# Kernel optimization log

Measured on AMD Instinct MI355X. Metric: run time of the kernel, lower is better.

## Reference

```python
import jax, jax.numpy as jnp
from jax import lax
import numpy as np

EPS = 1e-5

def _bn(y, g, b):
    # train-mode batchnorm over (B, H, W) per channel, biased variance (torch default)
    m = y.mean(axis=(0, 2, 3), keepdims=True)
    v = y.var(axis=(0, 2, 3), keepdims=True)
    return (y - m) * lax.rsqrt(v + EPS) * g[None, :, None, None] + b[None, :, None, None]

def _pool13(y):
    # max_pool2d kernel (13,1), stride (13,1); torch truncates the remainder
    B, Ch, L, C = y.shape
    L2 = (L // 13) * 13
    return y[:, :, :L2, :].reshape(B, Ch, L // 13, 13, C).max(axis=3)

def _stagenet(x, w1, b1, w2, b2, g1, be1, w3, b3, g2, be2, wl, bl):
    # x: (B, T=3000, C) -> (B, 100)
    B = x.shape[0]
    y = jnp.einsum('btc,oc->bot', x, w1) + b1[None, :, None]   # spatial conv across channels
    y = y.transpose(0, 2, 1)[:, None]                          # (B,1,T,C)
    y = lax.conv_general_dilated(y, w2, (1, 1), 'VALID', dimension_numbers=('NCHW', 'OIHW', 'NCHW')) + b2[None, :, None, None]
    y = _pool13(_bn(jax.nn.relu(y), g1, be1))                  # (B,16,227,C)
    y = lax.conv_general_dilated(y, w3, (1, 1), 'VALID', dimension_numbers=('NCHW', 'OIHW', 'NCHW')) + b3[None, :, None, None]
    y = _pool13(_bn(jax.nn.relu(y), g2, be2))                  # (B,16,13,C)
    return y.reshape(B, -1) @ wl.T + bl                        # (B,100)

def _gru_last(xs, wih, whh, bih, bhh):
    # xs: (B, S, D) -> final hidden state (B, H); torch gate order r, z, n
    h0 = jnp.zeros((xs.shape[0], whh.shape[1]), xs.dtype)
    def step(h, x):
        gi = x @ wih.T + bih
        gh = h @ whh.T + bhh
        ir, iz, inn = jnp.split(gi, 3, axis=-1)
        hr, hz, hnn = jnp.split(gh, 3, axis=-1)
        r = jax.nn.sigmoid(ir + hr)
        z = jax.nn.sigmoid(iz + hz)
        n = jnp.tanh(inn + r * hnn)
        return (1.0 - z) * n + z * h, None
    hT, _ = lax.scan(step, h0, xs.transpose(1, 0, 2))
    return hT

def setup_inputs() -> dict:
    key = jax.random.key(0)
    ks = jax.random.split(key, 16)
    B, Np, Nb, T, C, H = 16, 16, 10, 3000, 2, 100
    s = 0.1
    f32 = jnp.float32
    return {
        'Xc': jax.random.normal(ks[0], (B, Np, T, C), f32),
        'Xp': jax.random.normal(ks[1], (B, Np, T, C), f32),
        'Xb': jax.random.normal(ks[2], (B, Np, Nb, T, C), f32),
        'sn_w1': jax.random.normal(ks[3], (C, C), f32) * s,
        'sn_b1': jnp.zeros((C,), f32),
        'sn_w2': jax.random.normal(ks[4], (16, 1, 50, 1), f32) * s,
        'sn_b2': jnp.zeros((16,), f32),
        'sn_g1': jnp.ones((16,), f32),
        'sn_be1': jnp.zeros((16,), f32),
        'sn_w3': jax.random.normal(ks[5], (16, 16, 50, 1), f32) * s,
        'sn_b3': jnp.zeros((16,), f32),
        'sn_g2': jnp.ones((16,), f32),
        'sn_be2': jnp.zeros((16,), f32),
        'sn_wl': jax.random.normal(ks[6], (H, 16 * 13 * C), f32) * s,
        'sn_bl': jnp.zeros((H,), f32),
        'gru_wih': jax.random.normal(ks[7], (3 * H, H), f32) * s,
        'gru_whh': jax.random.normal(ks[8], (3 * H, H), f32) * s,
        'gru_bih': jnp.zeros((3 * H,), f32),
        'gru_bhh': jnp.zeros((3 * H,), f32),
        'bilin_w': jax.random.normal(ks[9], (Np, H, H), f32) * s,
    }

def reference(Xc, Xp, Xb, sn_w1, sn_b1, sn_w2, sn_b2, sn_g1, sn_be1, sn_w3, sn_b3, sn_g2, sn_be2, sn_wl, sn_bl, gru_wih, gru_whh, gru_bih, gru_bhh, bilin_w):
    sn = lambda x: _stagenet(x, sn_w1, sn_b1, sn_w2, sn_b2, sn_g1, sn_be1, sn_w3, sn_b3, sn_g2, sn_be2, sn_wl, sn_bl)
    B, Np, Nb, T, C = Xb.shape
    # each original stagenet call sees one window with batch B (BN stats per call) -> vmap over windows
    xb = jax.vmap(sn)(Xb.transpose(1, 2, 0, 3, 4).reshape(Np * Nb, B, T, C))
    xb = xb.reshape(Np, Nb, B, -1).transpose(2, 0, 1, 3)            # (B,Np,Nb,100)
    xc = jax.vmap(sn)(Xc.transpose(1, 0, 2, 3)).transpose(1, 0, 2)  # (B,S,100)
    xp = jax.vmap(sn)(Xp.transpose(1, 0, 2, 3)).transpose(1, 0, 2)  # (B,Np,100)
    hn = _gru_last(xc, gru_wih, gru_whh, gru_bih, gru_bhh)          # (B,100)
    cand = jnp.concatenate([xp[:, :, None, :], xb], axis=2)         # (B,Np,Nb+1,100)
    # per-step bilinear scoring: replaces the triple nested loop of nn.Bilinear calls
    return jnp.einsum('bh,phc,bpsc->bps', hn, bilin_w, cand)        # (B,16,11)
```

## Files before the change

kernel.cpp:

```cpp
#include <hip/hip_runtime.h>
#include <hip/hip_bf16.h>


#define NSEQ 3072
#define CNT1 94432.0f
#define CNT2 5696.0f

__global__ __launch_bounds__(256) void k0_prep(
    const float* __restrict__ wl, const float* __restrict__ w3,
    const float* __restrict__ wih, const float* __restrict__ whh,
    float* __restrict__ wlT, float* __restrict__ w3T,
    float* __restrict__ wihT, float* __restrict__ whhT)
{
    int i = blockIdx.x * 256 + threadIdx.x;
    if (i < 41600) { int h = i / 416, c = i - h * 416; wlT[c * 100 + h] = wl[i]; }
    if (i < 12800) { int co = i / 800, r = i - co * 800; int ci = r / 50, k = r - ci * 50;
                     w3T[(ci * 50 + k) * 16 + co] = w3[i]; }
    if (i < 30000) { int j = i / 100, c = i - j * 100;
                     wihT[c * 300 + j] = wih[i]; whhT[c * 300 + j] = whh[i]; }
}

__global__ __launch_bounds__(256) void k1(
    const float* __restrict__ Xc, const float* __restrict__ Xp, const float* __restrict__ Xb,
    const float* __restrict__ w1, const float* __restrict__ b1,
    const float* __restrict__ w2, const float* __restrict__ b2,
    const float* __restrict__ g1,
    float* __restrict__ pooled1, float* __restrict__ bp1)
{
    const int s = blockIdx.x;
    const int g = s >> 4, b = s & 15;
    const float* x;
    if (g < 160)      { int p = g / 10, nb = g - p * 10; x = Xb + (size_t)((b * 16 + p) * 10 + nb) * 6000; }
    else if (g < 176) { int p = g - 160; x = Xc + (size_t)(b * 16 + p) * 6000; }
    else              { int p = g - 176; x = Xp + (size_t)(b * 16 + p) * 6000; }

    __shared__ __align__(16) float u[6000];
    __shared__ float w2s[800];
    __shared__ float red[512];
    const int tid = threadIdx.x;

    for (int i = tid; i < 800; i += 256) w2s[i] = w2[i];
    float w100 = w1[0], w101 = w1[1], w110 = w1[2], w111 = w1[3];
    float b10 = b1[0], b11 = b1[1];
    for (int t4 = tid; t4 < 1500; t4 += 256) {
        float4 xv = ((const float4*)x)[t4];
        float4 uv;
        uv.x = fmaf(xv.y, w101, fmaf(xv.x, w100, b10));
        uv.y = fmaf(xv.y, w111, fmaf(xv.x, w110, b11));
        uv.z = fmaf(xv.w, w101, fmaf(xv.z, w100, b10));
        uv.w = fmaf(xv.w, w111, fmaf(xv.z, w110, b11));
        ((float4*)u)[t4] = uv;
    }
    __syncthreads();

    const int pair = tid & 31, ch = pair >> 1, col = pair & 1, w8 = tid >> 5;
    float wk[50];
    #pragma unroll
    for (int k = 0; k < 50; ++k) wk[k] = w2s[ch * 50 + k];
    #pragma unroll
    for (int k = 0; k < 50; ++k) asm volatile("" : "+v"(wk[k]));
    const float bias = b2[ch];
    const bool useMax = (g1[ch] >= 0.0f);

    float lsum = 0.0f, lsq = 0.0f;
    #pragma unroll 1
    for (int w = w8; w < 227; w += 8) {
        const int t0 = w * 13;
        float acc[13];
        #pragma unroll
        for (int j = 0; j < 13; ++j) acc[j] = bias;
        #pragma unroll
        for (int tk = 0; tk < 62; ++tk) {
            float uv = u[(t0 + tk) * 2 + col];
            const int jlo = (tk > 49) ? (tk - 49) : 0;
            const int jhi = (tk < 12) ? tk : 12;
            #pragma unroll
            for (int j = 0; j < 13; ++j)
                if (j >= jlo && j <= jhi) acc[j] = fmaf(uv, wk[tk - j], acc[j]);
        }
        float sel = useMax ? -1e30f : 1e30f;
        #pragma unroll
        for (int j = 0; j < 13; ++j) {
            float r = fmaxf(acc[j], 0.0f);
            lsum += r; lsq = fmaf(r, r, lsq);
            sel = useMax ? fmaxf(sel, r) : fminf(sel, r);
        }
        pooled1[(size_t)s * 7264 + (size_t)w * 32 + pair] = sel;
    }

    red[tid] = lsum;
    __syncthreads();
    float partial_sq = lsq;
    if (tid < 16) {
        float a = 0.0f;
        for (int t = 0; t < 16; ++t) { int idx = (t >> 1) * 32 + tid * 2 + (t & 1); a += red[idx]; }
        bp1[(s * 16 + tid) * 2 + 0] = a;
    }
    __syncthreads();
    red[tid] = partial_sq;
    __syncthreads();
    if (tid < 16) {
        float q = 0.0f;
        for (int t = 0; t < 16; ++t) { int idx = (t >> 1) * 32 + tid * 2 + (t & 1); q += red[idx]; }
        bp1[(s * 16 + tid) * 2 + 1] = q;
    }
}

__global__ __launch_bounds__(448) void k2(
    const float* __restrict__ pooled1, const float* __restrict__ bp1,
    const float* __restrict__ g1, const float* __restrict__ be1,
    const float* __restrict__ w3T, const float* __restrict__ b3,
    const float* __restrict__ g2,
    float* __restrict__ pooled2, float* __restrict__ bp2)
{
    const int s = blockIdx.x, g = s >> 4;
    __shared__ float in2[7424];
    __shared__ float w3b[2][800];
    __shared__ float sc1[16], sh1[16];
    __shared__ float red[896];
    const int tid = threadIdx.x;

    if (tid < 16) {
        float sum = 0.0f, sq = 0.0f;
        for (int sb = 0; sb < 16; ++sb) {
            const float* pp = &bp1[((g * 16 + sb) * 16 + tid) * 2];
            sum += pp[0]; sq += pp[1];
        }
        float m = sum * (1.0f / CNT1);
        float v = sq * (1.0f / CNT1) - m * m;
        float scv = g1[tid] * rsqrtf(v + 1e-5f);
        sc1[tid] = scv; sh1[tid] = be1[tid] - m * scv;
    }
    if (tid < 160) { int row = tid / 5, w = 227 + tid % 5; in2[row * 232 + w] = 0.0f; }
    for (int i = tid; i < 800; i += 448) w3b[0][i] = w3T[i];
    __syncthreads();
    for (int idx = tid; idx < 7264; idx += 448) {
        int w = idx >> 5, pr = idx & 31, ch = pr >> 1, cl = pr & 1;
        in2[(cl * 16 + ch) * 232 + w] = fmaf(pooled1[(size_t)s * 7264 + idx], sc1[ch], sh1[ch]);
    }

    const int pair = tid & 31, co = pair >> 1, col = pair & 1, wslot = tid >> 5;
    const int t0 = wslot * 13;
    float acc[13];
    const float bias = b3[co];
    #pragma unroll
    for (int j = 0; j < 13; ++j) acc[j] = bias;
    __syncthreads();

    for (int ci = 0; ci < 16; ++ci) {
        const int cur = ci & 1;
        if (ci < 15)
            for (int i = tid; i < 800; i += 448) w3b[cur ^ 1][i] = w3T[(ci + 1) * 800 + i];
        float wk[50];
        #pragma unroll
        for (int k = 0; k < 50; ++k) wk[k] = w3b[cur][k * 16 + co];
        #pragma unroll
        for (int k = 0; k < 50; ++k) asm volatile("" : "+v"(wk[k]));
        const float* ip = &in2[(col * 16 + ci) * 232 + t0];
        #pragma unroll
        for (int tk = 0; tk < 62; ++tk) {
            float uv = ip[tk];
            const int jlo = (tk > 49) ? (tk - 49) : 0;
            const int jhi = (tk < 12) ? tk : 12;
            #pragma unroll
            for (int j = 0; j < 13; ++j)
                if (j >= jlo && j <= jhi) acc[j] = fmaf(uv, wk[tk - j], acc[j]);
        }
        __syncthreads();
    }

    float lsum = 0.0f, lsq = 0.0f;
    const bool useMax2 = (g2[co] >= 0.0f);
    float sel = useMax2 ? -1e30f : 1e30f;
    {
        const int base = wslot * 13;
        #pragma unroll
        for (int j = 0; j < 13; ++j) {
            if (base + j < 178) {
                float r = fmaxf(acc[j], 0.0f);
                lsum += r; lsq = fmaf(r, r, lsq);
                sel = useMax2 ? fmaxf(sel, r) : fminf(sel, r);
            }
        }
        if (wslot < 13) pooled2[(size_t)s * 416 + co * 26 + wslot * 2 + col] = sel;
    }
    red[tid] = lsum; red[448 + tid] = lsq;
    __syncthreads();
    if (tid < 16) {
        float a = 0.0f, q = 0.0f;
        for (int t = 0; t < 28; ++t) {
            int idx = (t >> 1) * 32 + tid * 2 + (t & 1);
            a += red[idx]; q += red[448 + idx];
        }
        bp2[(s * 16 + tid) * 2 + 0] = a;
        bp2[(s * 16 + tid) * 2 + 1] = q;
    }
}

__global__ __launch_bounds__(128) void k3(
    const float* __restrict__ bp2, const float* __restrict__ g2, const float* __restrict__ be2,
    const float* __restrict__ pooled2, const float* __restrict__ wlT,
    const float* __restrict__ bl, float* __restrict__ feat)
{
    const int s = blockIdx.x, g = s >> 4;
    const int tid = threadIdx.x;
    __shared__ float sc[16], sh[16], z[416];
    if (tid < 16) {
        float sum = 0.0f, sq = 0.0f;
        for (int sb = 0; sb < 16; ++sb) {
            const float* pp = &bp2[((g * 16 + sb) * 16 + tid) * 2];
            sum += pp[0]; sq += pp[1];
        }
        float m = sum * (1.0f / CNT2);
        float v = sq * (1.0f / CNT2) - m * m;
        float scv = g2[tid] * rsqrtf(v + 1e-5f);
        sc[tid] = scv; sh[tid] = be2[tid] - m * scv;
    }
    __syncthreads();
    for (int i = tid; i < 416; i += 128) {
        int co = i / 26;
        z[i] = fmaf(pooled2[(size_t)s * 416 + i], sc[co], sh[co]);
    }
    __syncthreads();
    for (int h = tid; h < 100; h += 128) {
        float acc = bl[h];
        for (int i = 0; i < 416; ++i) acc = fmaf(wlT[i * 100 + h], z[i], acc);
        feat[(size_t)s * 100 + h] = acc;
    }
}

__global__ __launch_bounds__(128) void k4a(
    const float* __restrict__ feat, const float* __restrict__ wihT,
    const float* __restrict__ bih, float* __restrict__ gi)
{
    const int b = blockIdx.x >> 4, p = blockIdx.x & 15;
    const int tid = threadIdx.x;
    __shared__ float xr[100];
    if (tid < 100) xr[tid] = feat[(size_t)((160 + p) * 16 + b) * 100 + tid];
    __syncthreads();
    for (int j = tid; j < 300; j += 128) {
        float acc = bih[j];
        for (int i = 0; i < 100; ++i) acc = fmaf(xr[i], wihT[i * 300 + j], acc);
        gi[(size_t)(b * 16 + p) * 300 + j] = acc;
    }
}

__global__ __launch_bounds__(320) void k4b(
    const float* __restrict__ gi, const float* __restrict__ whhT,
    const float* __restrict__ bhh, float* __restrict__ hn)
{
    const int b = blockIdx.x;
    const int tid = threadIdx.x;
    __shared__ float h[100], ga[300], gb[300];
    if (tid < 100) h[tid] = 0.0f;
    __syncthreads();
    for (int p = 0; p < 16; ++p) {
        if (tid < 300) {
            float acc = bhh[tid];
            for (int i = 0; i < 100; ++i) acc = fmaf(h[i], whhT[i * 300 + tid], acc);
            gb[tid] = acc;
            ga[tid] = gi[(size_t)(b * 16 + p) * 300 + tid];
        }
        __syncthreads();
        if (tid < 100) {
            float r  = 1.0f / (1.0f + expf(-(ga[tid] + gb[tid])));
            float zz = 1.0f / (1.0f + expf(-(ga[100 + tid] + gb[100 + tid])));
            float n  = tanhf(ga[200 + tid] + r * gb[200 + tid]);
            h[tid] = (1.0f - zz) * n + zz * h[tid];
        }
        __syncthreads();
    }
    if (tid < 100) hn[b * 100 + tid] = h[tid];
}

__global__ __launch_bounds__(128) void k5(
    const float* __restrict__ hn, const float* __restrict__ bw,
    const float* __restrict__ feat, float* __restrict__ out)
{
    const int b = blockIdx.x >> 4, p = blockIdx.x & 15;
    const int tid = threadIdx.x;
    __shared__ float hs[100], ts[100];
    if (tid < 100) hs[tid] = hn[b * 100 + tid];
    __syncthreads();
    if (tid < 100) {
        float acc = 0.0f;
        for (int hh = 0; hh < 100; ++hh)
            acc = fmaf(hs[hh], bw[(size_t)(p * 100 + hh) * 100 + tid], acc);
        ts[tid] = acc;
    }
    __syncthreads();
    if (tid < 11) {
        const float* cr = (tid == 0)
            ? &feat[(size_t)((176 + p) * 16 + b) * 100]
            : &feat[(size_t)((p * 10 + tid - 1) * 16 + b) * 100];
        float acc = 0.0f;
        for (int hh = 0; hh < 100; ++hh) acc = fmaf(ts[hh], cr[hh], acc);
        out[(b * 16 + p) * 11 + tid] = acc;
    }
}

extern "C" void kernel_launch(void* const* d_in, const int* in_sizes, int n_in,
                              void* d_out, int out_size, void* d_ws, size_t ws_size,
                              hipStream_t stream) {
    (void)in_sizes; (void)n_in; (void)out_size; (void)ws_size;
    const float* Xc  = (const float*)d_in[0];
    const float* Xp  = (const float*)d_in[1];
    const float* Xb  = (const float*)d_in[2];
    const float* w1  = (const float*)d_in[3];
    const float* b1  = (const float*)d_in[4];
    const float* w2  = (const float*)d_in[5];
    const float* b2  = (const float*)d_in[6];
    const float* g1  = (const float*)d_in[7];
    const float* be1 = (const float*)d_in[8];
    const float* w3  = (const float*)d_in[9];
    const float* b3  = (const float*)d_in[10];
    const float* g2  = (const float*)d_in[11];
    const float* be2 = (const float*)d_in[12];
    const float* wl  = (const float*)d_in[13];
    const float* bl  = (const float*)d_in[14];
    const float* wih = (const float*)d_in[15];
    const float* whh = (const float*)d_in[16];
    const float* bih = (const float*)d_in[17];
    const float* bhh = (const float*)d_in[18];
    const float* bw  = (const float*)d_in[19];

    float* ws      = (float*)d_ws;
    float* bp1     = ws;
    float* bp2     = ws + 98304;
    float* wlT     = ws + 196608;
    float* w3T     = ws + 238208;
    float* wihT    = ws + 251008;
    float* whhT    = ws + 281008;
    float* gi      = ws + 311008;
    float* hn      = ws + 387808;
    float* feat    = ws + 389408;
    float* pooled2 = ws + 696608;
    float* pooled1 = ws + 1974560;

    k0_prep<<<163, 256, 0, stream>>>(wl, w3, wih, whh, wlT, w3T, wihT, whhT);
    k1<<<NSEQ, 256, 0, stream>>>(Xc, Xp, Xb, w1, b1, w2, b2, g1, pooled1, bp1);
    k2<<<NSEQ, 448, 0, stream>>>(pooled1, bp1, g1, be1, w3T, b3, g2, pooled2, bp2);
    k3<<<NSEQ, 128, 0, stream>>>(bp2, g2, be2, pooled2, wlT, bl, feat);
    k4a<<<256, 128, 0, stream>>>(feat, wihT, bih, gi);
    k4b<<<16, 320, 0, stream>>>(gi, whhT, bhh, hn);
    k5<<<256, 128, 0, stream>>>(hn, bw, feat, (float*)d_out);
}
```

Baseline: 804.4 us.

## Restructure k2 to 256 threads with two output windows per thread

The second conv kernel now runs with 256 threads instead of 448, and each thread computes up to two pooled windows (slot w8 and w8+8), so weights loaded into registers are reused across both windows. The transposed w3 layout becomes per-output-channel contiguous with padding to 52, which lets each thread read its 50 weights as a contiguous run from shared memory. The asm register-pinning barriers are dropped in k1 and k2, and k2 gets launch_bounds(256,2). This trades more per-thread register pressure and imbalance (only 6 of 8 warps do the second window) for fewer threads and better weight reuse.

```diff
diff --git a/kernel.cpp b/kernel.cpp
--- a/kernel.cpp
+++ b/kernel.cpp
@@ -15,7 +15,7 @@
     int i = blockIdx.x * 256 + threadIdx.x;
     if (i < 41600) { int h = i / 416, c = i - h * 416; wlT[c * 100 + h] = wl[i]; }
     if (i < 12800) { int co = i / 800, r = i - co * 800; int ci = r / 50, k = r - ci * 50;
-                     w3T[(ci * 50 + k) * 16 + co] = w3[i]; }
+                     w3T[ci * 832 + co * 52 + k] = w3[i]; }
     if (i < 30000) { int j = i / 100, c = i - j * 100;
                      wihT[c * 300 + j] = wih[i]; whhT[c * 300 + j] = whh[i]; }
 }
@@ -57,8 +57,6 @@
     float wk[50];
     #pragma unroll
     for (int k = 0; k < 50; ++k) wk[k] = w2s[ch * 50 + k];
-    #pragma unroll
-    for (int k = 0; k < 50; ++k) asm volatile("" : "+v"(wk[k]));
     const float bias = b2[ch];
     const bool useMax = (g1[ch] >= 0.0f);
 
@@ -106,7 +104,7 @@
     }
 }
 
-__global__ __launch_bounds__(448) void k2(
+__global__ __launch_bounds__(256, 2) void k2(
     const float* __restrict__ pooled1, const float* __restrict__ bp1,
     const float* __restrict__ g1, const float* __restrict__ be1,
     const float* __restrict__ w3T, const float* __restrict__ b3,
@@ -115,9 +113,9 @@
 {
     const int s = blockIdx.x, g = s >> 4;
     __shared__ float in2[7424];
-    __shared__ float w3b[2][800];
+    __shared__ __align__(16) float w3b[2][832];
     __shared__ float sc1[16], sh1[16];
-    __shared__ float red[896];
+    __shared__ float red[512];
     const int tid = threadIdx.x;
 
     if (tid < 16) {
@@ -132,65 +130,87 @@
         sc1[tid] = scv; sh1[tid] = be1[tid] - m * scv;
     }
     if (tid < 160) { int row = tid / 5, w = 227 + tid % 5; in2[row * 232 + w] = 0.0f; }
-    for (int i = tid; i < 800; i += 448) w3b[0][i] = w3T[i];
-    __syncthreads();
-    for (int idx = tid; idx < 7264; idx += 448) {
+    for (int i = tid; i < 832; i += 256) w3b[0][i] = w3T[i];
+    __syncthreads();
+    for (int idx = tid; idx < 7264; idx += 256) {
         int w = idx >> 5, pr = idx & 31, ch = pr >> 1, cl = pr & 1;
         in2[(cl * 16 + ch) * 232 + w] = fmaf(pooled1[(size_t)s * 7264 + idx], sc1[ch], sh1[ch]);
     }
 
-    const int pair = tid & 31, co = pair >> 1, col = pair & 1, wslot = tid >> 5;
-    const int t0 = wslot * 13;
-    float acc[13];
+    const int pair = tid & 31, co = pair >> 1, col = pair & 1, w8 = tid >> 5;
+    const bool hasB = (w8 < 6);
+    float accA[13], accB[13];
     const float bias = b3[co];
     #pragma unroll
-    for (int j = 0; j < 13; ++j) acc[j] = bias;
-    __syncthreads();
-
+    for (int j = 0; j < 13; ++j) { accA[j] = bias; accB[j] = bias; }
+    __syncthreads();
+
+    #pragma unroll 1
     for (int ci = 0; ci < 16; ++ci) {
         const int cur = ci & 1;
         if (ci < 15)
-            for (int i = tid; i < 800; i += 448) w3b[cur ^ 1][i] = w3T[(ci + 1) * 800 + i];
+            for (int i = tid; i < 832; i += 256) w3b[cur ^ 1][i] = w3T[(ci + 1) * 832 + i];
         float wk[50];
-        #pragma unroll
-        for (int k = 0; k < 50; ++k) wk[k] = w3b[cur][k * 16 + co];
-        #pragma unroll
-        for (int k = 0; k < 50; ++k) asm volatile("" : "+v"(wk[k]));
-        const float* ip = &in2[(col * 16 + ci) * 232 + t0];
+        const float* wp = &w3b[cur][co * 52];
+        #pragma unroll
+        for (int k = 0; k < 50; ++k) wk[k] = wp[k];
+        const float* ipA = &in2[(col * 16 + ci) * 232 + w8 * 13];
         #pragma unroll
         for (int tk = 0; tk < 62; ++tk) {
-            float uv = ip[tk];
+            float uv = ipA[tk];
             const int jlo = (tk > 49) ? (tk - 49) : 0;
             const int jhi = (tk < 12) ? tk : 12;
             #pragma unroll
             for (int j = 0; j < 13; ++j)
-                if (j >= jlo && j <= jhi) acc[j] = fmaf(uv, wk[tk - j], acc[j]);
+                if (j >= jlo && j <= jhi) accA[j] = fmaf(uv, wk[tk - j], accA[j]);
+        }
+        if (hasB) {
+            const float* ipB = ipA + 104;
+            #pragma unroll
+            for (int tk = 0; tk < 62; ++tk) {
+                float uv = ipB[tk];
+                const int jlo = (tk > 49) ? (tk - 49) : 0;
+                const int jhi = (tk < 12) ? tk : 12;
+                #pragma unroll
+                for (int j = 0; j < 13; ++j)
+                    if (j >= jlo && j <= jhi) accB[j] = fmaf(uv, wk[tk - j], accB[j]);
+            }
         }
         __syncthreads();
     }
 
     float lsum = 0.0f, lsq = 0.0f;
     const bool useMax2 = (g2[co] >= 0.0f);
-    float sel = useMax2 ? -1e30f : 1e30f;
     {
-        const int base = wslot * 13;
+        float sel = useMax2 ? -1e30f : 1e30f;
+        #pragma unroll
+        for (int j = 0; j < 13; ++j) {
+            float r = fmaxf(accA[j], 0.0f);
+            lsum += r; lsq = fmaf(r, r, lsq);
+            sel = useMax2 ? fmaxf(sel, r) : fminf(sel, r);
+        }
+        pooled2[(size_t)s * 416 + co * 26 + w8 * 2 + col] = sel;
+    }
+    if (hasB) {
+        const int slot = w8 + 8, base = slot * 13;
+        float sel = useMax2 ? -1e30f : 1e30f;
         #pragma unroll
         for (int j = 0; j < 13; ++j) {
             if (base + j < 178) {
-                float r = fmaxf(acc[j], 0.0f);
+                float r = fmaxf(accB[j], 0.0f);
                 lsum += r; lsq = fmaf(r, r, lsq);
                 sel = useMax2 ? fmaxf(sel, r) : fminf(sel, r);
             }
         }
-        if (wslot < 13) pooled2[(size_t)s * 416 + co * 26 + wslot * 2 + col] = sel;
-    }
-    red[tid] = lsum; red[448 + tid] = lsq;
+        if (slot < 13) pooled2[(size_t)s * 416 + co * 26 + slot * 2 + col] = sel;
+    }
+    red[tid] = lsum; red[256 + tid] = lsq;
     __syncthreads();
     if (tid < 16) {
         float a = 0.0f, q = 0.0f;
-        for (int t = 0; t < 28; ++t) {
+        for (int t = 0; t < 16; ++t) {
             int idx = (t >> 1) * 32 + tid * 2 + (t & 1);
-            a += red[idx]; q += red[448 + idx];
+            a += red[idx]; q += red[256 + idx];
         }
         bp2[(s * 16 + tid) * 2 + 0] = a;
         bp2[(s * 16 + tid) * 2 + 1] = q;
@@ -329,17 +349,17 @@
     float* bp2     = ws + 98304;
     float* wlT     = ws + 196608;
     float* w3T     = ws + 238208;
-    float* wihT    = ws + 251008;
-    float* whhT    = ws + 281008;
-    float* gi      = ws + 311008;
-    float* hn      = ws + 387808;
-    float* feat    = ws + 389408;
-    float* pooled2 = ws + 696608;
-    float* pooled1 = ws + 1974560;
+    float* wihT    = ws + 251520;
+    float* whhT    = ws + 281520;
+    float* gi      = ws + 311520;
+    float* hn      = ws + 388320;
+    float* feat    = ws + 389920;
+    float* pooled2 = ws + 697120;
+    float* pooled1 = ws + 1975072;
 
     k0_prep<<<163, 256, 0, stream>>>(wl, w3, wih, whh, wlT, w3T, wihT, whhT);
     k1<<<NSEQ, 256, 0, stream>>>(Xc, Xp, Xb, w1, b1, w2, b2, g1, pooled1, bp1);
-    k2<<<NSEQ, 448, 0, stream>>>(pooled1, bp1, g1, be1, w3T, b3, g2, pooled2, bp2);
+    k2<<<NSEQ, 256, 0, stream>>>(pooled1, bp1, g1, be1, w3T, b3, g2, pooled2, bp2);
     k3<<<NSEQ, 128, 0, stream>>>(bp2, g2, be2, pooled2, wlT, bl, feat);
     k4a<<<256, 128, 0, stream>>>(feat, wihT, bih, gi);
     k4b<<<16, 320, 0, stream>>>(gi, whhT, bhh, hn);
```

Measured after the change: 1.675 ms. +108.2%, slower.
